# Kernel optimization log

Measured on AMD Instinct MI355X. Metric: run time of the kernel, lower is better.

The kernel has to match this reference:

```python
import jax, jax.numpy as jnp
import numpy as np

SIGMA = 1.0


def _make_kps(key, B, NH, J, res):
    kx, ky, kv = jax.random.split(key, 3)
    xs = jax.random.randint(kx, (B, NH, J), 0, res)
    ys = jax.random.randint(ky, (B, NH, J), 0, res)
    vis = jax.random.randint(kv, (B, NH, J), 0, 2)
    kps = jnp.zeros((B, NH, 3 * J), dtype=jnp.int32)
    kps = kps.at[:, :, 0::3].set(xs.astype(jnp.int32))
    kps = kps.at[:, :, 1::3].set(ys.astype(jnp.int32))
    kps = kps.at[:, :, 2::3].set(vis.astype(jnp.int32))
    return kps


def setup_inputs() -> dict:
    key = jax.random.key(0)
    k0, k1, k2, k3 = jax.random.split(key, 4)
    B, NH, J = 8, 30, 17
    tag_maps0 = jax.random.normal(k0, (B, J, 256, 256), dtype=jnp.float32)
    tag_maps1 = jax.random.normal(k1, (B, J, 512, 512), dtype=jnp.float32)
    kps0 = _make_kps(k2, B, NH, J, 256)
    kps1 = _make_kps(k3, B, NH, J, 512)
    return {"tag_maps0": tag_maps0, "tag_maps1": tag_maps1, "kps0": kps0, "kps1": kps1}


def _single_ae_loss(kps, tmap, sigma=SIGMA):
    # kps: [NH, 3*J] int; tmap: [J, H, W] float
    J = tmap.shape[0]
    xs = kps[:, 0::3]              # [NH, J] row index into H
    ys = kps[:, 1::3]              # [NH, J] col index into W
    vis = kps[:, 2::3]             # [NH, J]
    jidx = jnp.arange(J)[None, :]
    vals = tmap[jidx, xs, ys]      # [NH, J] gathered tag values
    mask = (vis != 0).astype(tmap.dtype)
    cnt = mask.sum(-1)             # valid joints per human
    avg = (vals * mask).sum(-1) / jnp.maximum(cnt, 1.0)
    avg = jnp.where(cnt > 0, avg, 0.0)       # humans with no tags get avg 0
    num_humans = (cnt > 0).astype(tmap.dtype).sum()
    # pull loss: sum over valid joints of (tag - human_mean)^2, / num_humans
    pull = (((vals - avg[:, None]) * mask) ** 2).sum() / num_humans
    # push loss: full pairwise (incl. diagonal and zero-avg humans), / num_humans^2
    diff = avg[:, None] - avg[None, :]
    push = jnp.exp(-(diff ** 2) / (2.0 * sigma ** 2)).sum() / (num_humans ** 2)
    return pull + push


def reference(tag_maps0, tag_maps1, kps0, kps1):
    l0 = jax.vmap(_single_ae_loss)(kps0, tag_maps0)  # [B]
    l1 = jax.vmap(_single_ae_loss)(kps1, tag_maps1)  # [B]
    return l0 + l1
```

## Files before the change

### kernel.cpp

```cpp
#include <hip/hip_runtime.h>

static constexpr int J  = 17;
static constexpr int NH = 30;

__global__ __launch_bounds__(128) void ae_loss_kernel(
    const float* __restrict__ tm0,
    const float* __restrict__ tm1,
    const int*   __restrict__ kps0,
    const int*   __restrict__ kps1,
    float*       __restrict__ out)
{
    const int b    = blockIdx.x;
    const int wave = threadIdx.x >> 6;
    const int lane = threadIdx.x & 63;

    const int    res  = wave ? 512 : 256;
    const float* tmap = wave ? (tm1 + (size_t)b * J * 512 * 512)
                             : (tm0 + (size_t)b * J * 256 * 256);
    const int*   kps  = (wave ? kps1 : kps0) + b * NH * 3 * J;

    __shared__ float s_avg[2][NH];
    __shared__ float s_loss[2];

    float    vals[J];
    unsigned mbits = 0;
    float    avg   = 0.f;
    int      cnt   = 0;

    if (lane < NH) {
        const int* k = kps + lane * 3 * J;
        float sum = 0.f;
        #pragma unroll
        for (int j = 0; j < J; ++j) {
            const int x = k[3 * j + 0];
            const int y = k[3 * j + 1];
            const int v = k[3 * j + 2];
            const float val = tmap[((size_t)j * res + x) * res + y];
            vals[j] = val;
            if (v != 0) { mbits |= (1u << j); cnt++; sum += val; }
        }
        avg = (cnt > 0) ? (sum / (float)cnt) : 0.f;
        s_avg[wave][lane] = avg;
    }
    __syncthreads();

    float pull_h   = 0.f;
    float push_row = 0.f;
    float nh       = 0.f;
    if (lane < NH) {
        #pragma unroll
        for (int j = 0; j < J; ++j) {
            if (mbits & (1u << j)) {
                const float d = vals[j] - avg;
                pull_h += d * d;
            }
        }
        nh = (cnt > 0) ? 1.f : 0.f;
        #pragma unroll
        for (int m = 0; m < NH; ++m) {
            const float d = avg - s_avg[wave][m];
            push_row += expf(-0.5f * d * d);
        }
    }

    float psum = pull_h, qsum = push_row, nsum = nh;
    #pragma unroll
    for (int off = 32; off > 0; off >>= 1) {
        psum += __shfl_down(psum, off);
        qsum += __shfl_down(qsum, off);
        nsum += __shfl_down(nsum, off);
    }
    if (lane == 0) {
        const float inv = 1.f / nsum;
        s_loss[wave] = psum * inv + qsum * inv * inv;
    }
    __syncthreads();

    if (threadIdx.x == 0) out[b] = s_loss[0] + s_loss[1];
}

extern "C" void kernel_launch(void* const* d_in, const int* in_sizes, int n_in,
                              void* d_out, int out_size, void* d_ws, size_t ws_size,
                              hipStream_t stream) {
    const float* tm0  = (const float*)d_in[0];
    const float* tm1  = (const float*)d_in[1];
    const int*   kps0 = (const int*)d_in[2];
    const int*   kps1 = (const int*)d_in[3];
    float*       out  = (float*)d_out;

    const int B = in_sizes[2] / (NH * 3 * J);
    ae_loss_kernel<<<B, 128, 0, stream>>>(tm0, tm1, kps0, kps1, out);
}
```

Baseline: 9.373 us.

## Pack both scales into one wavefront and replace LDS sync with shuffles

Each block now uses a single 64-lane wavefront, with lanes 0-31 handling the 256 scale and lanes 32-63 the 512 scale. The per-human averages are shared through cross-lane shuffles rather than LDS, which removes both __syncthreads barriers and the shared-memory traffic. The reduction shrinks to 32-lane halves, the final sum moves through a shuffle, and expf becomes the faster __expf intrinsic. In exchange each block has half the threads, the gathers from both tag maps are issued by one wave, and the intrinsic is slightly less precise.

```diff
diff --git a/kernel.cpp b/kernel.cpp
--- a/kernel.cpp
+++ b/kernel.cpp
@@ -3,7 +3,7 @@
 static constexpr int J  = 17;
 static constexpr int NH = 30;
 
-__global__ __launch_bounds__(128) void ae_loss_kernel(
+__global__ __launch_bounds__(64) void ae_loss_kernel(
     const float* __restrict__ tm0,
     const float* __restrict__ tm1,
     const int*   __restrict__ kps0,
@@ -11,24 +11,22 @@
     float*       __restrict__ out)
 {
     const int b    = blockIdx.x;
-    const int wave = threadIdx.x >> 6;
-    const int lane = threadIdx.x & 63;
+    const int lane = threadIdx.x;
+    const int half = lane >> 5;
+    const int hl   = lane & 31;
 
-    const int    res  = wave ? 512 : 256;
-    const float* tmap = wave ? (tm1 + (size_t)b * J * 512 * 512)
+    const int    res  = half ? 512 : 256;
+    const float* tmap = half ? (tm1 + (size_t)b * J * 512 * 512)
                              : (tm0 + (size_t)b * J * 256 * 256);
-    const int*   kps  = (wave ? kps1 : kps0) + b * NH * 3 * J;
-
-    __shared__ float s_avg[2][NH];
-    __shared__ float s_loss[2];
+    const int*   kps  = (half ? kps1 : kps0) + b * NH * 3 * J;
 
     float    vals[J];
     unsigned mbits = 0;
     float    avg   = 0.f;
     int      cnt   = 0;
 
-    if (lane < NH) {
-        const int* k = kps + lane * 3 * J;
+    if (hl < NH) {
+        const int* k = kps + hl * 3 * J;
         float sum = 0.f;
         #pragma unroll
         for (int j = 0; j < J; ++j) {
@@ -40,43 +38,41 @@
             if (v != 0) { mbits |= (1u << j); cnt++; sum += val; }
         }
         avg = (cnt > 0) ? (sum / (float)cnt) : 0.f;
-        s_avg[wave][lane] = avg;
     }
-    __syncthreads();
 
-    float pull_h   = 0.f;
-    float push_row = 0.f;
-    float nh       = 0.f;
-    if (lane < NH) {
-        #pragma unroll
-        for (int j = 0; j < J; ++j) {
-            if (mbits & (1u << j)) {
-                const float d = vals[j] - avg;
-                pull_h += d * d;
-            }
-        }
-        nh = (cnt > 0) ? 1.f : 0.f;
-        #pragma unroll
-        for (int m = 0; m < NH; ++m) {
-            const float d = avg - s_avg[wave][m];
-            push_row += expf(-0.5f * d * d);
+    float pull_h = 0.f;
+    #pragma unroll
+    for (int j = 0; j < J; ++j) {
+        if (mbits & (1u << j)) {
+            const float d = vals[j] - avg;
+            pull_h = fmaf(d, d, pull_h);
         }
     }
 
+    float push_row = 0.f;
+    const int base = half << 5;
+    #pragma unroll
+    for (int m = 0; m < NH; ++m) {
+        const float am = __shfl(avg, base + m);
+        const float d  = avg - am;
+        push_row += __expf(-0.5f * d * d);
+    }
+    if (hl >= NH) { pull_h = 0.f; push_row = 0.f; }
+    const float nh = (hl < NH && cnt > 0) ? 1.f : 0.f;
+
     float psum = pull_h, qsum = push_row, nsum = nh;
     #pragma unroll
-    for (int off = 32; off > 0; off >>= 1) {
-        psum += __shfl_down(psum, off);
-        qsum += __shfl_down(qsum, off);
-        nsum += __shfl_down(nsum, off);
+    for (int off = 16; off > 0; off >>= 1) {
+        psum += __shfl_down(psum, off, 32);
+        qsum += __shfl_down(qsum, off, 32);
+        nsum += __shfl_down(nsum, off, 32);
     }
-    if (lane == 0) {
-        const float inv = 1.f / nsum;
-        s_loss[wave] = psum * inv + qsum * inv * inv;
-    }
-    __syncthreads();
 
-    if (threadIdx.x == 0) out[b] = s_loss[0] + s_loss[1];
+    const float inv = 1.f / nsum;
+    const float s   = fmaf(qsum * inv, inv, psum * inv);
+
+    const float s_other = __shfl(s, 32);
+    if (lane == 0) out[b] = s + s_other;
 }
 
 extern "C" void kernel_launch(void* const* d_in, const int* in_sizes, int n_in,
@@ -89,5 +85,5 @@
     float*       out  = (float*)d_out;
 
     const int B = in_sizes[2] / (NH * 3 * J);
-    ae_loss_kernel<<<B, 128, 0, stream>>>(tm0, tm1, kps0, kps1, out);
+    ae_loss_kernel<<<B, 64, 0, stream>>>(tm0, tm1, kps0, kps1, out);
 }
```

After: 9.387 us. Within noise of the previous version (+0.2%).
